# Performance work log

Hardware: AMD Instinct MI355X
Metric: run time of the kernel (lower is better)

## Reference

```python
import jax, jax.numpy as jnp
import numpy as np

N, E, XD, H, L, G, C = 20000, 320000, 128, 256, 4, 128, 10
EPS = 1e-5


def setup_inputs() -> dict:
    key = jax.random.key(0)
    ks = jax.random.split(key, 24)
    s = 0.05
    inp = {
        "x": jax.random.normal(ks[0], (N, XD), jnp.float32),
        "edge_index": jax.random.randint(ks[1], (2, E), 0, N, jnp.int32),
        "batch": jnp.sort(jax.random.randint(ks[2], (N,), 0, G, jnp.int32)),
        "encW": jax.random.normal(ks[3], (XD, H), jnp.float32) * s,
        "encB": jnp.zeros((H,), jnp.float32),
        "convW": jax.random.normal(ks[4], (L, H, H), jnp.float32) * s,
        "convB": jnp.zeros((L, H), jnp.float32),
        "bnG": jnp.ones((L, H), jnp.float32),
        "bnB": jnp.zeros((L, H), jnp.float32),
        "fcW1": jax.random.normal(ks[5], (H, H), jnp.float32) * s,
        "fcB1": jnp.zeros((H,), jnp.float32),
        "fcG1": jnp.ones((H,), jnp.float32),
        "fcBe1": jnp.zeros((H,), jnp.float32),
        "fcW2": jax.random.normal(ks[6], (H, H), jnp.float32) * s,
        "fcB2": jnp.zeros((H,), jnp.float32),
        "fcG2": jnp.ones((H,), jnp.float32),
        "fcBe2": jnp.zeros((H,), jnp.float32),
        "fcW3": jax.random.normal(ks[7], (H, C), jnp.float32) * s,
        "fcB3": jnp.zeros((C,), jnp.float32),
    }
    return inp


def _bn(h, g, b):
    # BatchNorm1d, training-mode batch statistics (biased var), eps=1e-5
    m = h.mean(0)
    v = h.var(0)
    return g * (h - m) * jax.lax.rsqrt(v + EPS) + b


def _forward(x, edge_index, batch, encW, encB, convW, convB, bnG, bnB,
             fcW1, fcB1, fcG1, fcBe1, fcW2, fcB2, fcG2, fcBe2, fcW3, fcB3):
    src, dst = edge_index[0], edge_index[1]
    # GCN symmetric normalization with implicit self-loops (fill value 1)
    deg = jax.ops.segment_sum(jnp.ones((E,), x.dtype), dst, num_segments=N) + 1.0
    dinv = jax.lax.rsqrt(deg)
    enorm = (dinv[src] * dinv[dst])[:, None]       # [E,1]
    self_norm = (dinv * dinv)[:, None]             # [N,1] self-loop coeff

    h = x @ encW + encB                            # node encoder
    for i in range(L):
        t = h @ convW[i]                           # GCNConv linear (no bias)
        agg = jax.ops.segment_sum(t[src] * enorm, dst, num_segments=N)
        t = agg + t * self_norm + convB[i]         # aggregate + self loop + bias
        h = jax.nn.relu(_bn(t, bnG[i], bnB[i]))    # dropout is identity (eval)

    # global mean pool over graph ids
    sums = jax.ops.segment_sum(h, batch, num_segments=G)
    cnts = jax.ops.segment_sum(jnp.ones((N,), h.dtype), batch, num_segments=G)
    g = sums / jnp.maximum(cnts, 1.0)[:, None]     # [G,H]

    # fc_out: MLP(Linear->BN->ReLU->Linear) -> BN -> Linear
    m = jax.nn.relu(_bn(g @ fcW1 + fcB1, fcG1, fcBe1)) @ fcW2 + fcB2
    m = _bn(m, fcG2, fcBe2)
    return m @ fcW3 + fcB3                         # [G,C]


def reference(x, edge_index, batch, encW, encB, convW, convB, bnG, bnB,
              fcW1, fcB1, fcG1, fcBe1, fcW2, fcB2, fcG2, fcBe2, fcW3, fcB3):
    return _forward(x, edge_index, batch, encW, encB, convW, convB, bnG, bnB,
                    fcW1, fcB1, fcG1, fcBe1, fcW2, fcB2, fcG2, fcBe2, fcW3, fcB3)
```

## Files before the change

kernel.cpp:

```cpp
#include <hip/hip_runtime.h>
#include <hip/hip_bf16.h>
#include <cstddef>

#define N_NODES 20000
#define N_EDGES 320000
#define XDIM 128
#define H 256
#define LAYERS 4
#define G_GRAPHS 128
#define C_OUT 10
#define EPS_BN 1e-5f
#define NSLOT 64
#define NB 8

typedef __attribute__((ext_vector_type(8))) short short8;
typedef __attribute__((ext_vector_type(4))) float f32x4;

__global__ void hist_kernel(const int* __restrict__ dst, int* __restrict__ cnt, int E) {
    int e = blockIdx.x * blockDim.x + threadIdx.x;
    if (e < E) atomicAdd(&cnt[dst[e]], 1);
}

__global__ void scan_kernel(const int* __restrict__ cnt, int* __restrict__ rowstart,
                            float* __restrict__ dinv, int N) {
    __shared__ int partial[1024];
    int tid = threadIdx.x;
    int chunk = (N + 1023) / 1024;
    int start = tid * chunk;
    int lsum = 0;
    for (int i = 0; i < chunk; ++i) {
        int idx = start + i;
        if (idx < N) {
            int c = cnt[idx];
            dinv[idx] = 1.0f / sqrtf((float)c + 1.0f);
            lsum += c;
        }
    }
    partial[tid] = lsum;
    __syncthreads();
    for (int off = 1; off < 1024; off <<= 1) {
        int v = (tid >= off) ? partial[tid - off] : 0;
        __syncthreads();
        partial[tid] += v;
        __syncthreads();
    }
    int run = (tid == 0) ? 0 : partial[tid - 1];
    for (int i = 0; i < chunk; ++i) {
        int idx = start + i;
        if (idx < N) { rowstart[idx] = run; run += cnt[idx]; }
    }
    if (tid == 1023) rowstart[N] = partial[1023];
}

__global__ void fill_kernel(const int* __restrict__ src, const int* __restrict__ dst,
                            const int* __restrict__ rowstart, int* __restrict__ cursor,
                            const float* __restrict__ dinv,
                            int* __restrict__ csr_src, float* __restrict__ csr_w, int E) {
    int e = blockIdx.x * blockDim.x + threadIdx.x;
    if (e < E) {
        int s = src[e], d = dst[e];
        int pos = rowstart[d] + atomicAdd(&cursor[d], 1);
        csr_src[pos] = s;
        csr_w[pos] = dinv[s] * dinv[d];
    }
}

__global__ void cast_bf16_kernel(const float* __restrict__ in, __hip_bfloat16* __restrict__ out, int n) {
    int i = blockIdx.x * blockDim.x + threadIdx.x;
    if (i < n) out[i] = __float2bfloat16(in[i]);
}

__global__ void tcast_kernel(const float* __restrict__ in, __hip_bfloat16* __restrict__ out,
                             int R, int C, int layers) {
    int i = blockIdx.x * blockDim.x + threadIdx.x;
    int per = R * C;
    if (i >= per * layers) return;
    int l = i / per, rem = i - l * per;
    int r = rem / C, c = rem - r * C;
    out[(size_t)l * per + (size_t)c * R + r] = __float2bfloat16(in[i]);
}

template <int K>
__global__ __launch_bounds__(256) void gemm_bf16_kernel(
    const __hip_bfloat16* __restrict__ A,
    const __hip_bfloat16* __restrict__ BT,
    const float* __restrict__ bias,
    __hip_bfloat16* __restrict__ Cbf,
    int M, int Nn) {
    __shared__ short As[64 * 32];
    __shared__ short Bs[128 * 32];
    const short* Ash = (const short*)A;
    const short* Bsh = (const short*)BT;
    int tid = threadIdx.x;
    int lane = tid & 63;
    int wave = tid >> 6;
    int quad = lane >> 4;
    int lr = lane & 15;
    int wm = (wave & 1) * 32;
    int wn = (wave >> 1) * 64;
    int Mblk = blockIdx.x * 64;
    int Nblk = blockIdx.y * 128;

    f32x4 acc[2][4];
#pragma unroll
    for (int i = 0; i < 2; ++i)
#pragma unroll
        for (int j = 0; j < 4; ++j) acc[i][j] = (f32x4){0.f, 0.f, 0.f, 0.f};

    for (int k0 = 0; k0 < K; k0 += 32) {
        {
            int row = tid >> 2;
            int qs = tid & 3;
            int qg = qs ^ ((row >> 1) & 3);
            int arow = Mblk + row; if (arow >= M) arow = M - 1;
            *(float4*)&As[row * 32 + qs * 8] =
                *(const float4*)(Ash + (size_t)arow * K + k0 + qg * 8);
        }
#pragma unroll
        for (int i = 0; i < 2; ++i) {
            int s = i * 256 + tid;
            int row = s >> 2;
            int qs = s & 3;
            int qg = qs ^ ((row >> 1) & 3);
            int brow = Nblk + row;
            *(float4*)&Bs[row * 32 + qs * 8] =
                *(const float4*)(Bsh + (size_t)brow * K + k0 + qg * 8);
        }
        __syncthreads();
        short8 af[2], bfr[4];
#pragma unroll
        for (int mi = 0; mi < 2; ++mi) {
            int r = wm + mi * 16 + lr;
            af[mi] = *(const short8*)&As[r * 32 + (quad ^ ((r >> 1) & 3)) * 8];
        }
#pragma unroll
        for (int ni = 0; ni < 4; ++ni) {
            int r = wn + ni * 16 + lr;
            bfr[ni] = *(const short8*)&Bs[r * 32 + (quad ^ ((r >> 1) & 3)) * 8];
        }
#pragma unroll
        for (int mi = 0; mi < 2; ++mi)
#pragma unroll
            for (int ni = 0; ni < 4; ++ni)
                acc[mi][ni] = __builtin_amdgcn_mfma_f32_16x16x32_bf16(af[mi], bfr[ni], acc[mi][ni], 0, 0, 0);
        __syncthreads();
    }
#pragma unroll
    for (int mi = 0; mi < 2; ++mi) {
#pragma unroll
        for (int r = 0; r < 4; ++r) {
            int m = Mblk + wm + mi * 16 + quad * 4 + r;
            if (m < M) {
#pragma unroll
                for (int ni = 0; ni < 4; ++ni) {
                    int n = Nblk + wn + ni * 16 + lr;
                    float v = acc[mi][ni][r];
                    if (bias) v += bias[n];
                    Cbf[(size_t)m * Nn + n] = __float2bfloat16(v);
                }
            }
        }
    }
}

__global__ __launch_bounds__(256) void agg_kernel(const __hip_bfloat16* __restrict__ t,
                           const int* __restrict__ rowstart,
                           const int* __restrict__ csr_src,
                           const float* __restrict__ csr_w,
                           const float* __restrict__ dinv,
                           const float* __restrict__ convB,
                           float* __restrict__ out,
                           float* __restrict__ spart,
                           int N) {
    __shared__ float red[4][256];
    int tid = threadIdx.x;
    int wave = tid >> 6;
    int lane = tid & 63;
    int sub = lane >> 5;
    int hl = lane & 31;
    int stream = wave * 2 + sub;
    int c0 = hl * 8;
    const ushort* tp = (const ushort*)t;
    float sv = 0.f, sq = 0.f;
    int n0 = blockIdx.x * NB;
#pragma unroll 1
    for (int it = 0; it < NB; ++it) {
        int n = n0 + it;
        int s = rowstart[n], e = rowstart[n + 1];
        float a[8] = {};
#pragma unroll 1
        for (int j0 = s; j0 < e; j0 += 16) {
#pragma unroll
            for (int u = 0; u < 2; ++u) {
                int j = j0 + u * 8 + stream;
                int idx = n; float w = 0.f;
                if (j < e) { idx = csr_src[j]; w = csr_w[j]; }
                uint4 v = *(const uint4*)(tp + (size_t)idx * H + c0);
                a[0] += __uint_as_float(v.x << 16) * w;
                a[1] += __uint_as_float(v.x & 0xffff0000u) * w;
                a[2] += __uint_as_float(v.y << 16) * w;
                a[3] += __uint_as_float(v.y & 0xffff0000u) * w;
                a[4] += __uint_as_float(v.z << 16) * w;
                a[5] += __uint_as_float(v.z & 0xffff0000u) * w;
                a[6] += __uint_as_float(v.w << 16) * w;
                a[7] += __uint_as_float(v.w & 0xffff0000u) * w;
            }
        }
#pragma unroll
        for (int k = 0; k < 8; ++k) a[k] += __shfl_xor(a[k], 32);
        if (sub == 0) {
            *(float4*)&red[wave][c0] = make_float4(a[0], a[1], a[2], a[3]);
            *(float4*)&red[wave][c0 + 4] = make_float4(a[4], a[5], a[6], a[7]);
        }
        __syncthreads();
        int c = tid;
        float val = red[0][c] + red[1][c] + red[2][c] + red[3][c];
        float dn = dinv[n];
        val += __bfloat162float(t[(size_t)n * H + c]) * (dn * dn) + convB[c];
        out[(size_t)n * H + c] = val;
        sv += val; sq += val * val;
        __syncthreads();
    }
    float* sp = spart + (size_t)(blockIdx.x & (NSLOT - 1)) * (2 * H);
    atomicAdd(&sp[tid], sv);
    atomicAdd(&sp[H + tid], sq);
}

__global__ void reduce_stats_kernel(const float* __restrict__ spart, float* __restrict__ stats) {
    int c = blockIdx.x * 256 + threadIdx.x;
    float s = 0.f;
#pragma unroll 8
    for (int i = 0; i < NSLOT; ++i) s += spart[(size_t)i * (2 * H) + c];
    stats[c] = s;
}

__global__ void bnrelu_kernel(const float* __restrict__ t, const float* __restrict__ stats,
                              const float* __restrict__ gamma, const float* __restrict__ beta,
                              __hip_bfloat16* __restrict__ out, int N) {
    int c = threadIdx.x;
    float invN = 1.0f / (float)N;
    float mean = stats[c] * invN;
    float var = stats[H + c] * invN - mean * mean;
    float sc = gamma[c] / sqrtf(var + EPS_BN);
    float sh = beta[c] - mean * sc;
    for (int r = blockIdx.x; r < N; r += gridDim.x) {
        float v = t[(size_t)r * H + c];
        out[(size_t)r * H + c] = __float2bfloat16(fmaxf(v * sc + sh, 0.f));
    }
}

__global__ __launch_bounds__(256) void pool_kernel(const __hip_bfloat16* __restrict__ h,
                            const int* __restrict__ batch,
                            float* __restrict__ g, int N) {
    __shared__ float4 red[4][64];
    int gid = blockIdx.x;
    int lo = 0, hi = N;
    while (lo < hi) { int mid = (lo + hi) >> 1; if (batch[mid] < gid) lo = mid + 1; else hi = mid; }
    int s = lo;
    lo = s; hi = N;
    while (lo < hi) { int mid = (lo + hi) >> 1; if (batch[mid] < gid + 1) lo = mid + 1; else hi = mid; }
    int e = lo;
    int wave = threadIdx.x >> 6;
    int lane = threadIdx.x & 63;
    const ushort* hp = (const ushort*)h;
    float a0 = 0.f, a1 = 0.f, a2 = 0.f, a3 = 0.f;
    for (int r = s + wave; r < e; r += 4) {
        uint2 v = *(const uint2*)(hp + (size_t)r * H + lane * 4);
        a0 += __uint_as_float(v.x << 16);
        a1 += __uint_as_float(v.x & 0xffff0000u);
        a2 += __uint_as_float(v.y << 16);
        a3 += __uint_as_float(v.y & 0xffff0000u);
    }
    red[wave][lane] = make_float4(a0, a1, a2, a3);
    __syncthreads();
    int c = threadIdx.x;
    const float* rf = (const float*)red;
    float sum = rf[c] + rf[256 + c] + rf[512 + c] + rf[768 + c];
    g[(size_t)gid * H + c] = sum / fmaxf((float)(e - s), 1.0f);
}

template <int K, int NN>
__global__ __launch_bounds__(256) void fc_lds_kernel(const float* __restrict__ in,
                                                     const float* __restrict__ W,
                                                     const float* __restrict__ b,
                                                     float* __restrict__ out) {
    __shared__ float row[K];
    int g = blockIdx.x;
    for (int k = threadIdx.x; k < K; k += 256) row[k] = in[(size_t)g * K + k];
    __syncthreads();
    int hc = threadIdx.x;
    if (hc < NN) {
        float acc = b[hc];
#pragma unroll
        for (int k = 0; k < K; ++k) acc += row[k] * W[k * NN + hc];
        out[(size_t)g * NN + hc] = acc;
    }
}

__global__ void fc_out_kernel(const float* __restrict__ in, const float* __restrict__ W,
                              const float* __restrict__ b, float* __restrict__ out) {
    int t = blockIdx.x * blockDim.x + threadIdx.x;
    if (t >= G_GRAPHS * C_OUT) return;
    int g = t / C_OUT, c = t % C_OUT;
    float acc = b[c];
#pragma unroll 16
    for (int k = 0; k < H; ++k) acc += in[(size_t)g * H + k] * W[k * C_OUT + c];
    out[t] = acc;
}

__global__ void bn_head_kernel(const float* __restrict__ in, const float* __restrict__ gamma,
                               const float* __restrict__ beta, float* __restrict__ out,
                               int Grows, int relu) {
    int c = blockIdx.x;
    int r = threadIdx.x;
    __shared__ float red[G_GRAPHS];
    float v = in[r * H + c];
    red[r] = v;
    __syncthreads();
    for (int off = G_GRAPHS / 2; off > 0; off >>= 1) {
        if (r < off) red[r] += red[r + off];
        __syncthreads();
    }
    float mean = red[0] / (float)Grows;
    __syncthreads();
    float d = v - mean;
    red[r] = d * d;
    __syncthreads();
    for (int off = G_GRAPHS / 2; off > 0; off >>= 1) {
        if (r < off) red[r] += red[r + off];
        __syncthreads();
    }
    float var = red[0] / (float)Grows;
    float y = gamma[c] * d / sqrtf(var + EPS_BN) + beta[c];
    if (relu) y = fmaxf(y, 0.f);
    out[r * H + c] = y;
}

extern "C" void kernel_launch(void* const* d_in, const int* in_sizes, int n_in,
                              void* d_out, int out_size, void* d_ws, size_t ws_size,
                              hipStream_t stream) {
    const float* x     = (const float*)d_in[0];
    const int*   edge  = (const int*)d_in[1];
    const int*   batch = (const int*)d_in[2];
    const float* encW  = (const float*)d_in[3];
    const float* encB  = (const float*)d_in[4];
    const float* convW = (const float*)d_in[5];
    const float* convB = (const float*)d_in[6];
    const float* bnG   = (const float*)d_in[7];
    const float* bnB   = (const float*)d_in[8];
    const float* fcW1  = (const float*)d_in[9];
    const float* fcB1  = (const float*)d_in[10];
    const float* fcG1  = (const float*)d_in[11];
    const float* fcBe1 = (const float*)d_in[12];
    const float* fcW2  = (const float*)d_in[13];
    const float* fcB2  = (const float*)d_in[14];
    const float* fcG2  = (const float*)d_in[15];
    const float* fcBe2 = (const float*)d_in[16];
    const float* fcW3  = (const float*)d_in[17];
    const float* fcB3  = (const float*)d_in[18];
    float* out = (float*)d_out;

    const int* srcIdx = edge;
    const int* dstIdx = edge + N_EDGES;

    char* base = (char*)d_ws;
    size_t off = 0;
    auto alloc = [&](size_t bytes) -> void* {
        void* p = base + off;
        off = (off + bytes + 255) & ~(size_t)255;
        return p;
    };
    int*   cnt      = (int*)alloc(N_NODES * 4);
    int*   cursor   = (int*)alloc(N_NODES * 4);
    int*   rowstart = (int*)alloc((N_NODES + 1) * 4);
    float* dinv     = (float*)alloc(N_NODES * 4);
    int*   csr_src  = (int*)alloc(N_EDGES * 4);
    float* csr_w    = (float*)alloc(N_EDGES * 4);
    float* bnstats  = (float*)alloc(LAYERS * 2 * H * 4);
    float* spart    = (float*)alloc((size_t)LAYERS * NSLOT * 2 * H * 4);
    __hip_bfloat16* xbf    = (__hip_bfloat16*)alloc((size_t)N_NODES * XDIM * 2);
    __hip_bfloat16* encWT  = (__hip_bfloat16*)alloc((size_t)H * XDIM * 2);
    __hip_bfloat16* convWT = (__hip_bfloat16*)alloc((size_t)LAYERS * H * H * 2);
    __hip_bfloat16* hbf    = (__hip_bfloat16*)alloc((size_t)N_NODES * H * 2);
    __hip_bfloat16* tbf    = (__hip_bfloat16*)alloc((size_t)N_NODES * H * 2);
    float* t2buf = (float*)alloc((size_t)N_NODES * H * 4);
    float* gpool = (float*)alloc(G_GRAPHS * H * 4);
    float* m1    = (float*)alloc(G_GRAPHS * H * 4);
    float* m2    = (float*)alloc(G_GRAPHS * H * 4);

    hipMemsetAsync(cnt, 0, N_NODES * 4, stream);
    hipMemsetAsync(cursor, 0, N_NODES * 4, stream);
    hipMemsetAsync(spart, 0, (size_t)LAYERS * NSLOT * 2 * H * 4, stream);

    hist_kernel<<<(N_EDGES + 255) / 256, 256, 0, stream>>>(dstIdx, cnt, N_EDGES);
    scan_kernel<<<1, 1024, 0, stream>>>(cnt, rowstart, dinv, N_NODES);
    fill_kernel<<<(N_EDGES + 255) / 256, 256, 0, stream>>>(srcIdx, dstIdx, rowstart, cursor,
                                                           dinv, csr_src, csr_w, N_EDGES);

    cast_bf16_kernel<<<(N_NODES * XDIM + 255) / 256, 256, 0, stream>>>(x, xbf, N_NODES * XDIM);
    tcast_kernel<<<(XDIM * H + 255) / 256, 256, 0, stream>>>(encW, encWT, XDIM, H, 1);
    tcast_kernel<<<(LAYERS * H * H + 255) / 256, 256, 0, stream>>>(convW, convWT, H, H, LAYERS);

    dim3 gridG((N_NODES + 63) / 64, H / 128);
    gemm_bf16_kernel<XDIM><<<gridG, 256, 0, stream>>>(xbf, encWT, encB, hbf, N_NODES, H);

    for (int l = 0; l < LAYERS; ++l) {
        float* spartL = spart + (size_t)l * NSLOT * 2 * H;
        gemm_bf16_kernel<H><<<gridG, 256, 0, stream>>>(hbf, convWT + (size_t)l * H * H, nullptr,
                                                       tbf, N_NODES, H);
        agg_kernel<<<N_NODES / NB, 256, 0, stream>>>(tbf, rowstart, csr_src, csr_w, dinv,
                                                     convB + l * H, t2buf, spartL, N_NODES);
        reduce_stats_kernel<<<2, 256, 0, stream>>>(spartL, bnstats + l * 2 * H);
        bnrelu_kernel<<<512, H, 0, stream>>>(t2buf, bnstats + l * 2 * H,
                                             bnG + l * H, bnB + l * H, hbf, N_NODES);
    }

    pool_kernel<<<G_GRAPHS, 256, 0, stream>>>(hbf, batch, gpool, N_NODES);

    fc_lds_kernel<H, H><<<G_GRAPHS, 256, 0, stream>>>(gpool, fcW1, fcB1, m1);
    bn_head_kernel<<<H, G_GRAPHS, 0, stream>>>(m1, fcG1, fcBe1, m1, G_GRAPHS, 1);
    fc_lds_kernel<H, H><<<G_GRAPHS, 256, 0, stream>>>(m1, fcW2, fcB2, m2);
    bn_head_kernel<<<H, G_GRAPHS, 0, stream>>>(m2, fcG2, fcBe2, m2, G_GRAPHS, 0);
    fc_out_kernel<<<(G_GRAPHS * C_OUT + 255) / 256, 256, 0, stream>>>(m2, fcW3, fcB3, out);
}
```

Baseline: 493.9 us.

## Fuse BatchNorm+ReLU into next GEMM A-load and pool; use direct global-to-LDS loads

Drops the standalone bnrelu pass. The BN scale/shift is now computed once per layer in a tiny kernel, then applied with ReLU and bf16 conversion while the following GEMM loads its fp32 A tile, and while the final pooling kernel reads its rows. This removes a full write and re-read of the bf16 activation buffer each layer. The cost is that the GEMM reads fp32 activations, which doubles A-side traffic. B tiles, and A tiles in the unfused case, now use global_load_lds direct-to-LDS transfers. Two memsets are also merged into one.

```diff
diff --git a/kernel.cpp b/kernel.cpp
--- a/kernel.cpp
+++ b/kernel.cpp
@@ -15,6 +15,8 @@
 
 typedef __attribute__((ext_vector_type(8))) short short8;
 typedef __attribute__((ext_vector_type(4))) float f32x4;
+typedef __attribute__((address_space(3))) unsigned int lds_u32;
+typedef const __attribute__((address_space(1))) unsigned int glob_u32;
 
 __global__ void hist_kernel(const int* __restrict__ dst, int* __restrict__ cnt, int E) {
     int e = blockIdx.x * blockDim.x + threadIdx.x;
@@ -80,16 +82,24 @@
     out[(size_t)l * per + (size_t)c * R + r] = __float2bfloat16(in[i]);
 }
 
-template <int K>
+__device__ __forceinline__ short bf16bits(float x) {
+    __hip_bfloat16 b = __float2bfloat16(x);
+    return *(short*)&b;
+}
+
+template <int K, bool FUSE_BN>
 __global__ __launch_bounds__(256) void gemm_bf16_kernel(
-    const __hip_bfloat16* __restrict__ A,
+    const void* __restrict__ Ain,
     const __hip_bfloat16* __restrict__ BT,
     const float* __restrict__ bias,
+    const float* __restrict__ bnsc,
+    const float* __restrict__ bnsh,
     __hip_bfloat16* __restrict__ Cbf,
     int M, int Nn) {
     __shared__ short As[64 * 32];
     __shared__ short Bs[128 * 32];
-    const short* Ash = (const short*)A;
+    const short* Ash = (const short*)Ain;
+    const float* Af = (const float*)Ain;
     const short* Bsh = (const short*)BT;
     int tid = threadIdx.x;
     int lane = tid & 63;
@@ -107,24 +117,41 @@
 #pragma unroll
         for (int j = 0; j < 4; ++j) acc[i][j] = (f32x4){0.f, 0.f, 0.f, 0.f};
 
+    int srow = tid >> 2, sqs = tid & 3;
+    int sqg = sqs ^ ((srow >> 1) & 3);
+    int arow = Mblk + srow; if (arow >= M) arow = M - 1;
+    int s1 = 256 + tid;
+    int brow0 = Nblk + (tid >> 2);
+    int qg0 = sqg;
+    int brow1 = Nblk + (s1 >> 2);
+    int qg1 = (s1 & 3) ^ (((s1 >> 2) >> 1) & 3);
+
     for (int k0 = 0; k0 < K; k0 += 32) {
-        {
-            int row = tid >> 2;
-            int qs = tid & 3;
-            int qg = qs ^ ((row >> 1) & 3);
-            int arow = Mblk + row; if (arow >= M) arow = M - 1;
-            *(float4*)&As[row * 32 + qs * 8] =
-                *(const float4*)(Ash + (size_t)arow * K + k0 + qg * 8);
-        }
-#pragma unroll
-        for (int i = 0; i < 2; ++i) {
-            int s = i * 256 + tid;
-            int row = s >> 2;
-            int qs = s & 3;
-            int qg = qs ^ ((row >> 1) & 3);
-            int brow = Nblk + row;
-            *(float4*)&Bs[row * 32 + qs * 8] =
-                *(const float4*)(Bsh + (size_t)brow * K + k0 + qg * 8);
+        int kc = k0 + sqg * 8;
+        __builtin_amdgcn_global_load_lds((glob_u32*)(Bsh + (size_t)brow0 * K + k0 + qg0 * 8),
+                                         (lds_u32*)Bs + wave * 256, 16, 0, 0);
+        __builtin_amdgcn_global_load_lds((glob_u32*)(Bsh + (size_t)brow1 * K + k0 + qg1 * 8),
+                                         (lds_u32*)Bs + 1024 + wave * 256, 16, 0, 0);
+        if (FUSE_BN) {
+            float4 v0 = *(const float4*)(Af + (size_t)arow * K + kc);
+            float4 v1 = *(const float4*)(Af + (size_t)arow * K + kc + 4);
+            float4 c0 = *(const float4*)(bnsc + kc);
+            float4 c1 = *(const float4*)(bnsc + kc + 4);
+            float4 h0 = *(const float4*)(bnsh + kc);
+            float4 h1 = *(const float4*)(bnsh + kc + 4);
+            short8 pk;
+            pk[0] = bf16bits(fmaxf(v0.x * c0.x + h0.x, 0.f));
+            pk[1] = bf16bits(fmaxf(v0.y * c0.y + h0.y, 0.f));
+            pk[2] = bf16bits(fmaxf(v0.z * c0.z + h0.z, 0.f));
+            pk[3] = bf16bits(fmaxf(v0.w * c0.w + h0.w, 0.f));
+            pk[4] = bf16bits(fmaxf(v1.x * c1.x + h1.x, 0.f));
+            pk[5] = bf16bits(fmaxf(v1.y * c1.y + h1.y, 0.f));
+            pk[6] = bf16bits(fmaxf(v1.z * c1.z + h1.z, 0.f));
+            pk[7] = bf16bits(fmaxf(v1.w * c1.w + h1.w, 0.f));
+            *(short8*)&As[srow * 32 + sqs * 8] = pk;
+        } else {
+            __builtin_amdgcn_global_load_lds((glob_u32*)(Ash + (size_t)arow * K + kc),
+                                             (lds_u32*)As + wave * 256, 16, 0, 0);
         }
         __syncthreads();
         short8 af[2], bfr[4];
@@ -226,31 +253,28 @@
     atomicAdd(&sp[H + tid], sq);
 }
 
-__global__ void reduce_stats_kernel(const float* __restrict__ spart, float* __restrict__ stats) {
-    int c = blockIdx.x * 256 + threadIdx.x;
-    float s = 0.f;
+__global__ void make_bnparams_kernel(const float* __restrict__ spart,
+                                     const float* __restrict__ gamma,
+                                     const float* __restrict__ beta,
+                                     float* __restrict__ sc, float* __restrict__ sh) {
+    int c = threadIdx.x;
+    float s = 0.f, s2 = 0.f;
 #pragma unroll 8
-    for (int i = 0; i < NSLOT; ++i) s += spart[(size_t)i * (2 * H) + c];
-    stats[c] = s;
-}
-
-__global__ void bnrelu_kernel(const float* __restrict__ t, const float* __restrict__ stats,
-                              const float* __restrict__ gamma, const float* __restrict__ beta,
-                              __hip_bfloat16* __restrict__ out, int N) {
-    int c = threadIdx.x;
-    float invN = 1.0f / (float)N;
-    float mean = stats[c] * invN;
-    float var = stats[H + c] * invN - mean * mean;
-    float sc = gamma[c] / sqrtf(var + EPS_BN);
-    float sh = beta[c] - mean * sc;
-    for (int r = blockIdx.x; r < N; r += gridDim.x) {
-        float v = t[(size_t)r * H + c];
-        out[(size_t)r * H + c] = __float2bfloat16(fmaxf(v * sc + sh, 0.f));
-    }
-}
-
-__global__ __launch_bounds__(256) void pool_kernel(const __hip_bfloat16* __restrict__ h,
+    for (int i = 0; i < NSLOT; ++i) {
+        s  += spart[(size_t)i * (2 * H) + c];
+        s2 += spart[(size_t)i * (2 * H) + H + c];
+    }
+    float invN = 1.0f / (float)N_NODES;
+    float mean = s * invN;
+    float var = s2 * invN - mean * mean;
+    float k = gamma[c] / sqrtf(var + EPS_BN);
+    sc[c] = k;
+    sh[c] = beta[c] - mean * k;
+}
+
+__global__ __launch_bounds__(256) void pool_kernel(const float* __restrict__ t2,
                             const int* __restrict__ batch,
+                            const float* __restrict__ sc, const float* __restrict__ sh,
                             float* __restrict__ g, int N) {
     __shared__ float4 red[4][64];
     int gid = blockIdx.x;
@@ -262,14 +286,15 @@
     int e = lo;
     int wave = threadIdx.x >> 6;
     int lane = threadIdx.x & 63;
-    const ushort* hp = (const ushort*)h;
+    float4 scv = *(const float4*)(sc + lane * 4);
+    float4 shv = *(const float4*)(sh + lane * 4);
     float a0 = 0.f, a1 = 0.f, a2 = 0.f, a3 = 0.f;
     for (int r = s + wave; r < e; r += 4) {
-        uint2 v = *(const uint2*)(hp + (size_t)r * H + lane * 4);
-        a0 += __uint_as_float(v.x << 16);
-        a1 += __uint_as_float(v.x & 0xffff0000u);
-        a2 += __uint_as_float(v.y << 16);
-        a3 += __uint_as_float(v.y & 0xffff0000u);
+        float4 v = *(const float4*)(t2 + (size_t)r * H + lane * 4);
+        a0 += __bfloat162float(__float2bfloat16(fmaxf(v.x * scv.x + shv.x, 0.f)));
+        a1 += __bfloat162float(__float2bfloat16(fmaxf(v.y * scv.y + shv.y, 0.f)));
+        a2 += __bfloat162float(__float2bfloat16(fmaxf(v.z * scv.z + shv.z, 0.f)));
+        a3 += __bfloat162float(__float2bfloat16(fmaxf(v.w * scv.w + shv.w, 0.f)));
     }
     red[wave][lane] = make_float4(a0, a1, a2, a3);
     __syncthreads();
@@ -376,8 +401,9 @@
     float* dinv     = (float*)alloc(N_NODES * 4);
     int*   csr_src  = (int*)alloc(N_EDGES * 4);
     float* csr_w    = (float*)alloc(N_EDGES * 4);
-    float* bnstats  = (float*)alloc(LAYERS * 2 * H * 4);
     float* spart    = (float*)alloc((size_t)LAYERS * NSLOT * 2 * H * 4);
+    float* scbuf    = (float*)alloc((size_t)LAYERS * H * 4);
+    float* shbuf    = (float*)alloc((size_t)LAYERS * H * 4);
     __hip_bfloat16* xbf    = (__hip_bfloat16*)alloc((size_t)N_NODES * XDIM * 2);
     __hip_bfloat16* encWT  = (__hip_bfloat16*)alloc((size_t)H * XDIM * 2);
     __hip_bfloat16* convWT = (__hip_bfloat16*)alloc((size_t)LAYERS * H * H * 2);
@@ -388,8 +414,7 @@
     float* m1    = (float*)alloc(G_GRAPHS * H * 4);
     float* m2    = (float*)alloc(G_GRAPHS * H * 4);
 
-    hipMemsetAsync(cnt, 0, N_NODES * 4, stream);
-    hipMemsetAsync(cursor, 0, N_NODES * 4, stream);
+    hipMemsetAsync(cnt, 0, (size_t)((char*)rowstart - (char*)cnt), stream);
     hipMemsetAsync(spart, 0, (size_t)LAYERS * NSLOT * 2 * H * 4, stream);
 
     hist_kernel<<<(N_EDGES + 255) / 256, 256, 0, stream>>>(dstIdx, cnt, N_EDGES);
@@ -402,20 +427,28 @@
     tcast_kernel<<<(LAYERS * H * H + 255) / 256, 256, 0, stream>>>(convW, convWT, H, H, LAYERS);
 
     dim3 gridG((N_NODES + 63) / 64, H / 128);
-    gemm_bf16_kernel<XDIM><<<gridG, 256, 0, stream>>>(xbf, encWT, encB, hbf, N_NODES, H);
+    gemm_bf16_kernel<XDIM, false><<<gridG, 256, 0, stream>>>(
+        xbf, encWT, encB, nullptr, nullptr, hbf, N_NODES, H);
 
     for (int l = 0; l < LAYERS; ++l) {
         float* spartL = spart + (size_t)l * NSLOT * 2 * H;
-        gemm_bf16_kernel<H><<<gridG, 256, 0, stream>>>(hbf, convWT + (size_t)l * H * H, nullptr,
-                                                       tbf, N_NODES, H);
+        if (l == 0) {
+            gemm_bf16_kernel<H, false><<<gridG, 256, 0, stream>>>(
+                hbf, convWT + (size_t)l * H * H, nullptr, nullptr, nullptr, tbf, N_NODES, H);
+        } else {
+            gemm_bf16_kernel<H, true><<<gridG, 256, 0, stream>>>(
+                t2buf, convWT + (size_t)l * H * H, nullptr,
+                scbuf + (size_t)(l - 1) * H, shbuf + (size_t)(l - 1) * H, tbf, N_NODES, H);
+        }
         agg_kernel<<<N_NODES / NB, 256, 0, stream>>>(tbf, rowstart, csr_src, csr_w, dinv,
                                                      convB + l * H, t2buf, spartL, N_NODES);
-        reduce_stats_kernel<<<2, 256, 0, stream>>>(spartL, bnstats + l * 2 * H);
-        bnrelu_kernel<<<512, H, 0, stream>>>(t2buf, bnstats + l * 2 * H,
-                                             bnG + l * H, bnB + l * H, hbf, N_NODES);
-    }
-
-    pool_kernel<<<G_GRAPHS, 256, 0, stream>>>(hbf, batch, gpool, N_NODES);
+        make_bnparams_kernel<<<1, H, 0, stream>>>(spartL, bnG + l * H, bnB + l * H,
+                                                  scbuf + (size_t)l * H, shbuf + (size_t)l * H);
+    }
+
+    pool_kernel<<<G_GRAPHS, 256, 0, stream>>>(t2buf, batch,
+                                              scbuf + (size_t)(LAYERS - 1) * H,
+                                              shbuf + (size_t)(LAYERS - 1) * H, gpool, N_NODES);
 
     fc_lds_kernel<H, H><<<G_GRAPHS, 256, 0, stream>>>(gpool, fcW1, fcB1, m1);
     bn_head_kernel<<<H, G_GRAPHS, 0, stream>>>(m1, fcG1, fcBe1, m1, G_GRAPHS, 1);
```

New measurement: 453.4 us. -8.2%, faster.
